# Kernel tuning notes

Measured on AMD Instinct MI355X. Metric: run time of the kernel, lower is better.

Reference implementation:

```python
import jax, jax.numpy as jnp
import numpy as np

B, N, E = 32, 1024, 768
H = 12
D = E // H  # head_dim = 64


def setup_inputs() -> dict:
    key = jax.random.key(0)
    ks = jax.random.split(key, 5)
    s = 0.02
    return {
        "x": jax.random.normal(ks[0], (B, N, E), dtype=jnp.float32),
        "w_qkv": jax.random.normal(ks[1], (E, 3 * E), dtype=jnp.float32) * s,
        "b_qkv": jax.random.normal(ks[2], (3 * E,), dtype=jnp.float32) * s,
        "w_proj": jax.random.normal(ks[3], (E, E), dtype=jnp.float32) * s,
        "b_proj": jax.random.normal(ks[4], (E,), dtype=jnp.float32) * s,
    }


def reference(x, w_qkv, b_qkv, w_proj, b_proj):
    b, n, e = x.shape
    # QKV projection -> [b, n, 3, H, D]
    qkv = (jnp.einsum('bne,ef->bnf', x, w_qkv) + b_qkv).reshape(b, n, 3, H, D)
    q = qkv[:, :, 0]  # [b, n, H, D]
    k = qkv[:, :, 1]
    v = qkv[:, :, 2]
    scale = 1.0 / jnp.sqrt(jnp.asarray(D, dtype=x.dtype))
    # attention scores [b, H, n, n]
    attn = jnp.einsum('bqhd,bkhd->bhqk', q, k) * scale
    attn = jax.nn.softmax(attn, axis=-1)
    # weighted values -> [b, n, H, D] -> [b, n, e]
    out = jnp.einsum('bhqk,bkhd->bqhd', attn, v).reshape(b, n, e)
    out = jnp.einsum('bne,ef->bnf', out, w_proj) + b_proj
    return out
```

## Files before the change

kernel.cpp:

```cpp
#include <hip/hip_runtime.h>
#include <hip/hip_bf16.h>
#include <stdint.h>

#define HB 12

typedef unsigned short u16;
typedef __bf16 bf16x8 __attribute__((ext_vector_type(8)));
typedef float f32x4 __attribute__((ext_vector_type(4)));
typedef float f4v __attribute__((ext_vector_type(4)));
typedef u16 u16x4 __attribute__((ext_vector_type(4)));
typedef u16 u16x8 __attribute__((ext_vector_type(8)));

__device__ __forceinline__ u16 f2bf(float f) {
  uint32_t u = __builtin_bit_cast(uint32_t, f);
  u += 0x7fffu + ((u >> 16) & 1u);
  return (u16)(u >> 16);
}

__device__ __forceinline__ void gld16(const u16* g, u16* l) {
  __builtin_amdgcn_global_load_lds((const __attribute__((address_space(1))) void*)g,
                                   (__attribute__((address_space(3))) void*)l, 16, 0, 0);
}

__device__ __forceinline__ f32x4 mfma_bf16(bf16x8 a, bf16x8 b, f32x4 c) {
  return __builtin_amdgcn_mfma_f32_16x16x32_bf16(a, b, c, 0, 0, 0);
}

__global__ void k_convert(const float* __restrict__ in, u16* __restrict__ out, int n4) {
  int stride = gridDim.x * blockDim.x;
  for (int i = blockIdx.x * blockDim.x + threadIdx.x; i < n4; i += stride) {
    f4v v = ((const f4v*)in)[i];
    u16x4 o;
    o[0] = f2bf(v[0]); o[1] = f2bf(v[1]); o[2] = f2bf(v[2]); o[3] = f2bf(v[3]);
    ((u16x4*)out)[i] = o;
  }
}

__global__ void k_transpose(const float* __restrict__ in, u16* __restrict__ out,
                            int rows, int cols) {
  __shared__ float t[32][33];
  int c0 = blockIdx.x * 32, r0 = blockIdx.y * 32;
  int tx = threadIdx.x, ty = threadIdx.y;
  for (int i = ty; i < 32; i += 8)
    t[i][tx] = in[(size_t)(r0 + i) * cols + c0 + tx];
  __syncthreads();
  for (int i = ty; i < 32; i += 8)
    out[(size_t)(c0 + i) * rows + r0 + tx] = f2bf(t[tx][i]);
}

template <int OUTF32>
__global__ void k_gemm(const u16* __restrict__ A, const u16* __restrict__ Bt,
                       const float* __restrict__ bias, void* __restrict__ C,
                       int Nc, int nx) {
  const int K = 768;
  __shared__ u16 lA[2][4096], lB[2][4096];
  int tid = threadIdx.x, w = tid >> 6, l = tid & 63;
  int lg = l >> 4, lr = l & 15;
  int wr = w >> 1, wc = w & 1;
  int lin = blockIdx.x;
  int xcd = lin & 7, idx = lin >> 3;
  int by = xcd * 32 + idx / nx;
  int bx = idx % nx;
  int m0 = by * 128, n0 = bx * 128;

  auto stage = [&](int buf, int k0) {
#pragma unroll
    for (int it = 0; it < 2; ++it) {
      int chunk = it * 256 + tid;
      int row = chunk >> 2, c = chunk & 3;
      int cg = (c ^ ((row >> 1) & 3)) * 8;
      gld16(&A[(size_t)(m0 + row) * K + k0 + cg], &lA[buf][chunk * 8]);
      gld16(&Bt[(size_t)(n0 + row) * K + k0 + cg], &lB[buf][chunk * 8]);
    }
  };

  f32x4 acc[4][4] = {};
  stage(0, 0);
  for (int kt = 0; kt < 24; ++kt) {
    __syncthreads();
    if (kt < 23) stage((kt + 1) & 1, (kt + 1) * 32);
    const u16* a = lA[kt & 1];
    const u16* b = lB[kt & 1];
    bf16x8 af[4], bfr[4];
#pragma unroll
    for (int i = 0; i < 4; ++i) {
      int ra = wr * 64 + i * 16 + lr;
      af[i] = *(const bf16x8*)&a[ra * 32 + ((lg ^ ((ra >> 1) & 3)) * 8)];
      int rb = wc * 64 + i * 16 + lr;
      bfr[i] = *(const bf16x8*)&b[rb * 32 + ((lg ^ ((rb >> 1) & 3)) * 8)];
    }
    __builtin_amdgcn_s_setprio(1);
#pragma unroll
    for (int i = 0; i < 4; ++i)
#pragma unroll
      for (int j = 0; j < 4; ++j)
        acc[i][j] = mfma_bf16(af[i], bfr[j], acc[i][j]);
    __builtin_amdgcn_s_setprio(0);
  }
#pragma unroll
  for (int j = 0; j < 4; ++j) {
    int col = n0 + wc * 64 + j * 16 + lr;
    float bv = bias[col];
#pragma unroll
    for (int i = 0; i < 4; ++i) {
      int rb = m0 + wr * 64 + i * 16 + lg * 4;
#pragma unroll
      for (int r = 0; r < 4; ++r) {
        float v = acc[i][j][r] + bv;
        if (OUTF32)
          ((float*)C)[(size_t)(rb + r) * Nc + col] = v;
        else
          ((u16*)C)[(size_t)(rb + r) * Nc + col] = f2bf(v);
      }
    }
  }
}

__global__ void k_vtrans(const u16* __restrict__ qkv, u16* __restrict__ vt) {
  __shared__ u16 t[64][80];
  int tid = threadIdx.x;
  int n0 = blockIdx.x * 64, bh = blockIdx.y;
  int b = bh / HB, h = bh % HB;
#pragma unroll
  for (int it = 0; it < 2; ++it) {
    int nl = it * 32 + (tid >> 3), dv0 = (tid & 7) * 8;
    u16x8 v = *(const u16x8*)&qkv[(size_t)(b * 1024 + n0 + nl) * 2304 + 1536 + h * 64 + dv0];
    *(u16x8*)&t[nl][dv0] = v;
  }
  __syncthreads();
  int dv = tid >> 2, c = (tid & 3) * 16;
  u16x8 o0, o1;
#pragma unroll
  for (int j = 0; j < 8; ++j) o0[j] = t[c + j][dv];
#pragma unroll
  for (int j = 0; j < 8; ++j) o1[j] = t[c + 8 + j][dv];
  size_t base = (size_t)(bh * 64 + dv) * 1024 + n0 + c;
  *(u16x8*)&vt[base] = o0;
  *(u16x8*)&vt[base + 8] = o1;
}

__global__ __launch_bounds__(256) void k_attn(const u16* __restrict__ qkv,
                                              const u16* __restrict__ vt,
                                              u16* __restrict__ out) {
  __shared__ u16 lK[2][4096];
  __shared__ u16 lV[2][4096];
  __shared__ u16 lP[8192];
  int tid = threadIdx.x, w = tid >> 6, l = tid & 63;
  int lg = l >> 4, lr = l & 15;
  int lin = blockIdx.x;
  int xcd = lin & 7, idx = lin >> 3;
  int bh = xcd * 48 + (idx >> 3);
  int qt = idx & 7;
  int b = bh / HB, h = bh % HB;
  int q0 = qt * 128;

#pragma unroll
  for (int it = 0; it < 4; ++it) {
    int chunk = it * 256 + tid;
    int row = chunk >> 3, c = chunk & 7;
    int cg = (c ^ (row & 7)) * 8;
    gld16(&qkv[(size_t)(b * 1024 + q0 + row) * 2304 + h * 64 + cg], &lP[chunk * 8]);
  }

  auto stage = [&](int buf, int kt) {
    int n0 = kt * 64;
#pragma unroll
    for (int it = 0; it < 2; ++it) {
      int chunk = it * 256 + tid;
      int row = chunk >> 3, c = chunk & 7;
      int cg = (c ^ (row & 7)) * 8;
      gld16(&qkv[(size_t)(b * 1024 + n0 + row) * 2304 + 768 + h * 64 + cg], &lK[buf][chunk * 8]);
      gld16(&vt[(size_t)(bh * 64 + row) * 1024 + n0 + cg], &lV[buf][chunk * 8]);
    }
  };

  stage(0, 0);
  __syncthreads();

  bf16x8 qf[2][2];
#pragma unroll
  for (int m = 0; m < 2; ++m)
#pragma unroll
    for (int kb = 0; kb < 2; ++kb) {
      int row = w * 32 + m * 16 + lr;
      qf[m][kb] = *(const bf16x8*)&lP[row * 64 + (((kb * 4 + lg) ^ (row & 7)) * 8)];
    }

  f32x4 oacc[2][4] = {};
  float mrun[2][4], lrun[2][4];
#pragma unroll
  for (int m = 0; m < 2; ++m)
#pragma unroll
    for (int j = 0; j < 4; ++j) { mrun[m][j] = -3.0e38f; lrun[m][j] = 0.f; }

  u16* Pw = &lP[w * 2048];
  const float scale = 0.125f;

  for (int kt = 0; kt < 16; ++kt) {
    int cur = kt & 1;
    if (kt < 15) stage(cur ^ 1, kt + 1);
    const u16* Kc = lK[cur];
    const u16* Vc = lV[cur];

    f32x4 sacc[2][4] = {};
    __builtin_amdgcn_s_setprio(1);
#pragma unroll
    for (int nf = 0; nf < 4; ++nf) {
      int rk = nf * 16 + lr;
      bf16x8 k0 = *(const bf16x8*)&Kc[rk * 64 + ((lg ^ (rk & 7)) * 8)];
      bf16x8 k1 = *(const bf16x8*)&Kc[rk * 64 + (((4 + lg) ^ (rk & 7)) * 8)];
      sacc[0][nf] = mfma_bf16(qf[0][0], k0, sacc[0][nf]);
      sacc[0][nf] = mfma_bf16(qf[0][1], k1, sacc[0][nf]);
      sacc[1][nf] = mfma_bf16(qf[1][0], k0, sacc[1][nf]);
      sacc[1][nf] = mfma_bf16(qf[1][1], k1, sacc[1][nf]);
    }
    __builtin_amdgcn_s_setprio(0);

#pragma unroll
    for (int m = 0; m < 2; ++m) {
#pragma unroll
      for (int j = 0; j < 4; ++j) {
        float tmax = -3.0e38f;
#pragma unroll
        for (int nf = 0; nf < 4; ++nf) {
          sacc[m][nf][j] *= scale;
          tmax = fmaxf(tmax, sacc[m][nf][j]);
        }
        tmax = fmaxf(tmax, __shfl_xor(tmax, 1));
        tmax = fmaxf(tmax, __shfl_xor(tmax, 2));
        tmax = fmaxf(tmax, __shfl_xor(tmax, 4));
        tmax = fmaxf(tmax, __shfl_xor(tmax, 8));
        float mnew = fmaxf(mrun[m][j], tmax);
        float corr = __expf(mrun[m][j] - mnew);
        float rsum = 0.f;
#pragma unroll
        for (int nf = 0; nf < 4; ++nf) {
          float p = __expf(sacc[m][nf][j] - mnew);
          sacc[m][nf][j] = p;
          rsum += p;
        }
        rsum += __shfl_xor(rsum, 1);
        rsum += __shfl_xor(rsum, 2);
        rsum += __shfl_xor(rsum, 4);
        rsum += __shfl_xor(rsum, 8);
        lrun[m][j] = lrun[m][j] * corr + rsum;
        mrun[m][j] = mnew;
#pragma unroll
        for (int dvf = 0; dvf < 4; ++dvf) oacc[m][dvf][j] *= corr;
      }
    }

#pragma unroll
    for (int m = 0; m < 2; ++m)
#pragma unroll
      for (int nf = 0; nf < 4; ++nf)
#pragma unroll
        for (int j = 0; j < 4; ++j) {
          int row = m * 16 + lg * 4 + j;
          int col = nf * 16 + lr;
          Pw[row * 64 + (((col >> 3) ^ (row & 7)) * 8) + (col & 7)] = f2bf(sacc[m][nf][j]);
        }

    __builtin_amdgcn_s_setprio(1);
#pragma unroll
    for (int kb2 = 0; kb2 < 2; ++kb2) {
      bf16x8 pf0, pf1;
      {
        int c = kb2 * 4 + lg;
        int r0r = lr;
        pf0 = *(const bf16x8*)&Pw[r0r * 64 + ((c ^ (r0r & 7)) * 8)];
        int r1r = 16 + lr;
        pf1 = *(const bf16x8*)&Pw[r1r * 64 + ((c ^ (r1r & 7)) * 8)];
      }
#pragma unroll
      for (int dvf = 0; dvf < 4; ++dvf) {
        int rv = dvf * 16 + lr, c = kb2 * 4 + lg;
        bf16x8 vf = *(const bf16x8*)&Vc[rv * 64 + ((c ^ (rv & 7)) * 8)];
        oacc[0][dvf] = mfma_bf16(pf0, vf, oacc[0][dvf]);
        oacc[1][dvf] = mfma_bf16(pf1, vf, oacc[1][dvf]);
      }
    }
    __builtin_amdgcn_s_setprio(0);

    if (kt < 15) __syncthreads();
  }

#pragma unroll
  for (int m = 0; m < 2; ++m)
#pragma unroll
    for (int j = 0; j < 4; ++j) {
      float inv = 1.f / lrun[m][j];
      int q = q0 + w * 32 + m * 16 + lg * 4 + j;
#pragma unroll
      for (int dvf = 0; dvf < 4; ++dvf) {
        int dv = dvf * 16 + lr;
        out[(size_t)(b * 1024 + q) * 768 + h * 64 + dv] = f2bf(oacc[m][dvf][j] * inv);
      }
    }
}

extern "C" void kernel_launch(void* const* d_in, const int* in_sizes, int n_in,
                              void* d_out, int out_size, void* d_ws, size_t ws_size,
                              hipStream_t stream) {
  const float* x      = (const float*)d_in[0];
  const float* w_qkv  = (const float*)d_in[1];
  const float* b_qkv  = (const float*)d_in[2];
  const float* w_proj = (const float*)d_in[3];
  const float* b_proj = (const float*)d_in[4];

  u16* ws = (u16*)d_ws;
  u16* xbf    = ws;
  u16* attn_o = xbf;
  u16* wqkvT  = ws + 25165824;
  u16* wprojT = wqkvT + 1769472;
  u16* qkvb   = wprojT + 589824;
  u16* vtb    = qkvb + 75497472;

  k_convert<<<2048, 256, 0, stream>>>(x, xbf, 25165824 / 4);
  k_transpose<<<dim3(2304 / 32, 768 / 32), dim3(32, 8), 0, stream>>>(w_qkv, wqkvT, 768, 2304);
  k_transpose<<<dim3(768 / 32, 768 / 32), dim3(32, 8), 0, stream>>>(w_proj, wprojT, 768, 768);
  k_gemm<0><<<18 * 256, 256, 0, stream>>>(xbf, wqkvT, b_qkv, qkvb, 2304, 18);
  k_vtrans<<<dim3(16, 384), 256, 0, stream>>>(qkvb, vtb);
  k_attn<<<3072, 256, 0, stream>>>(qkvb, vtb, attn_o);
  k_gemm<1><<<6 * 256, 256, 0, stream>>>(attn_o, wprojT, b_proj, d_out, 768, 6);
}
```

Before: 720.3 us.

## Switch attention to 32x32 MFMA with transposed S, keep P in registers

After: 584.2 us. -18.9%, faster.

```diff
diff --git a/kernel.cpp b/kernel.cpp
--- a/kernel.cpp
+++ b/kernel.cpp
@@ -5,17 +5,24 @@
 #define HB 12
 
 typedef unsigned short u16;
+typedef unsigned int u32;
 typedef __bf16 bf16x8 __attribute__((ext_vector_type(8)));
 typedef float f32x4 __attribute__((ext_vector_type(4)));
+typedef float f32x16 __attribute__((ext_vector_type(16)));
 typedef float f4v __attribute__((ext_vector_type(4)));
 typedef u16 u16x4 __attribute__((ext_vector_type(4)));
 typedef u16 u16x8 __attribute__((ext_vector_type(8)));
+typedef u32 u32x2 __attribute__((ext_vector_type(2)));
+typedef u32 u32x4v __attribute__((ext_vector_type(4)));
 
 __device__ __forceinline__ u16 f2bf(float f) {
   uint32_t u = __builtin_bit_cast(uint32_t, f);
   u += 0x7fffu + ((u >> 16) & 1u);
   return (u16)(u >> 16);
 }
+__device__ __forceinline__ u32 pack2bf(float lo, float hi) {
+  return (u32)f2bf(lo) | ((u32)f2bf(hi) << 16);
+}
 
 __device__ __forceinline__ void gld16(const u16* g, u16* l) {
   __builtin_amdgcn_global_load_lds((const __attribute__((address_space(1))) void*)g,
@@ -24,6 +31,9 @@
 
 __device__ __forceinline__ f32x4 mfma_bf16(bf16x8 a, bf16x8 b, f32x4 c) {
   return __builtin_amdgcn_mfma_f32_16x16x32_bf16(a, b, c, 0, 0, 0);
+}
+__device__ __forceinline__ f32x16 mfma32(bf16x8 a, bf16x8 b, f32x16 c) {
+  return __builtin_amdgcn_mfma_f32_32x32x16_bf16(a, b, c, 0, 0, 0);
 }
 
 __global__ void k_convert(const float* __restrict__ in, u16* __restrict__ out, int n4) {
@@ -139,27 +149,25 @@
   *(u16x8*)&vt[base + 8] = o1;
 }
 
-__global__ __launch_bounds__(256) void k_attn(const u16* __restrict__ qkv,
-                                              const u16* __restrict__ vt,
-                                              u16* __restrict__ out) {
+__global__ __launch_bounds__(256, 4) void k_attn(const u16* __restrict__ qkv,
+                                                 const u16* __restrict__ vt,
+                                                 u16* __restrict__ out) {
   __shared__ u16 lK[2][4096];
   __shared__ u16 lV[2][4096];
-  __shared__ u16 lP[8192];
   int tid = threadIdx.x, w = tid >> 6, l = tid & 63;
-  int lg = l >> 4, lr = l & 15;
+  int q32 = l & 31, hi = l >> 5;
   int lin = blockIdx.x;
   int xcd = lin & 7, idx = lin >> 3;
   int bh = xcd * 48 + (idx >> 3);
   int qt = idx & 7;
   int b = bh / HB, h = bh % HB;
-  int q0 = qt * 128;
-
-#pragma unroll
-  for (int it = 0; it < 4; ++it) {
-    int chunk = it * 256 + tid;
-    int row = chunk >> 3, c = chunk & 7;
-    int cg = (c ^ (row & 7)) * 8;
-    gld16(&qkv[(size_t)(b * 1024 + q0 + row) * 2304 + h * 64 + cg], &lP[chunk * 8]);
+  int qg = qt * 128 + w * 32 + q32;
+
+  bf16x8 qf[4];
+  {
+    const u16* qrow = &qkv[(size_t)(b * 1024 + qg) * 2304 + h * 64 + hi * 8];
+#pragma unroll
+    for (int ds = 0; ds < 4; ++ds) qf[ds] = *(const bf16x8*)&qrow[ds * 16];
   }
 
   auto stage = [&](int buf, int kt) {
@@ -177,24 +185,8 @@
   stage(0, 0);
   __syncthreads();
 
-  bf16x8 qf[2][2];
-#pragma unroll
-  for (int m = 0; m < 2; ++m)
-#pragma unroll
-    for (int kb = 0; kb < 2; ++kb) {
-      int row = w * 32 + m * 16 + lr;
-      qf[m][kb] = *(const bf16x8*)&lP[row * 64 + (((kb * 4 + lg) ^ (row & 7)) * 8)];
-    }
-
-  f32x4 oacc[2][4] = {};
-  float mrun[2][4], lrun[2][4];
-#pragma unroll
-  for (int m = 0; m < 2; ++m)
-#pragma unroll
-    for (int j = 0; j < 4; ++j) { mrun[m][j] = -3.0e38f; lrun[m][j] = 0.f; }
-
-  u16* Pw = &lP[w * 2048];
-  const float scale = 0.125f;
+  f32x16 oacc[2] = {};
+  float mrun = -3.0e38f, lrun = 0.f;
 
   for (int kt = 0; kt < 16; ++kt) {
     int cur = kt & 1;
@@ -202,100 +194,86 @@
     const u16* Kc = lK[cur];
     const u16* Vc = lV[cur];
 
-    f32x4 sacc[2][4] = {};
+    f32x16 s0 = {}, s1 = {};
     __builtin_amdgcn_s_setprio(1);
 #pragma unroll
-    for (int nf = 0; nf < 4; ++nf) {
-      int rk = nf * 16 + lr;
-      bf16x8 k0 = *(const bf16x8*)&Kc[rk * 64 + ((lg ^ (rk & 7)) * 8)];
-      bf16x8 k1 = *(const bf16x8*)&Kc[rk * 64 + (((4 + lg) ^ (rk & 7)) * 8)];
-      sacc[0][nf] = mfma_bf16(qf[0][0], k0, sacc[0][nf]);
-      sacc[0][nf] = mfma_bf16(qf[0][1], k1, sacc[0][nf]);
-      sacc[1][nf] = mfma_bf16(qf[1][0], k0, sacc[1][nf]);
-      sacc[1][nf] = mfma_bf16(qf[1][1], k1, sacc[1][nf]);
+    for (int ds = 0; ds < 4; ++ds) {
+      int dchunk = ds * 2 + hi;
+      int r0 = q32;
+      bf16x8 k0 = *(const bf16x8*)&Kc[r0 * 64 + ((dchunk ^ (r0 & 7)) * 8)];
+      int r1 = 32 + q32;
+      bf16x8 k1 = *(const bf16x8*)&Kc[r1 * 64 + ((dchunk ^ (r1 & 7)) * 8)];
+      s0 = mfma32(k0, qf[ds], s0);
+      s1 = mfma32(k1, qf[ds], s1);
     }
     __builtin_amdgcn_s_setprio(0);
 
-#pragma unroll
-    for (int m = 0; m < 2; ++m) {
-#pragma unroll
-      for (int j = 0; j < 4; ++j) {
-        float tmax = -3.0e38f;
-#pragma unroll
-        for (int nf = 0; nf < 4; ++nf) {
-          sacc[m][nf][j] *= scale;
-          tmax = fmaxf(tmax, sacc[m][nf][j]);
+    float tmax = -3.0e38f;
+#pragma unroll
+    for (int r = 0; r < 16; ++r) { s0[r] *= 0.125f; tmax = fmaxf(tmax, s0[r]); }
+#pragma unroll
+    for (int r = 0; r < 16; ++r) { s1[r] *= 0.125f; tmax = fmaxf(tmax, s1[r]); }
+    tmax = fmaxf(tmax, __shfl_xor(tmax, 32));
+
+    float mnew = fmaxf(mrun, tmax);
+    float corr = __expf(mrun - mnew);
+    lrun *= corr;
+#pragma unroll
+    for (int r = 0; r < 16; ++r) { oacc[0][r] *= corr; oacc[1][r] *= corr; }
+    mrun = mnew;
+
+    float rsum = 0.f;
+#pragma unroll
+    for (int r = 0; r < 16; ++r) { float p = __expf(s0[r] - mnew); s0[r] = p; rsum += p; }
+#pragma unroll
+    for (int r = 0; r < 16; ++r) { float p = __expf(s1[r] - mnew); s1[r] = p; rsum += p; }
+    lrun += rsum + __shfl_xor(rsum, 32);
+
+    __builtin_amdgcn_s_setprio(1);
+#pragma unroll
+    for (int half = 0; half < 2; ++half) {
+      const f32x16& pv = half ? s1 : s0;
+#pragma unroll
+      for (int u = 0; u < 2; ++u) {
+        int ns = half * 2 + u;
+        u32 a0 = pack2bf(pv[8 * u + 0], pv[8 * u + 1]);
+        u32 a1 = pack2bf(pv[8 * u + 2], pv[8 * u + 3]);
+        u32 a2 = pack2bf(pv[8 * u + 4], pv[8 * u + 5]);
+        u32 a3 = pack2bf(pv[8 * u + 6], pv[8 * u + 7]);
+        u32 pa0 = (u32)__shfl_xor((int)a0, 32);
+        u32 pa1 = (u32)__shfl_xor((int)a1, 32);
+        u32 pa2 = (u32)__shfl_xor((int)a2, 32);
+        u32 pa3 = (u32)__shfl_xor((int)a3, 32);
+        u32x4v pw;
+        pw[0] = hi ? pa2 : a0;
+        pw[1] = hi ? pa3 : a1;
+        pw[2] = hi ? a2 : pa0;
+        pw[3] = hi ? a3 : pa1;
+        bf16x8 pfrag = __builtin_bit_cast(bf16x8, pw);
+        int nchunk = ns * 2 + hi;
+#pragma unroll
+        for (int dt = 0; dt < 2; ++dt) {
+          int rv = dt * 32 + q32;
+          bf16x8 vf = *(const bf16x8*)&Vc[rv * 64 + ((nchunk ^ (rv & 7)) * 8)];
+          oacc[dt] = mfma32(vf, pfrag, oacc[dt]);
         }
-        tmax = fmaxf(tmax, __shfl_xor(tmax, 1));
-        tmax = fmaxf(tmax, __shfl_xor(tmax, 2));
-        tmax = fmaxf(tmax, __shfl_xor(tmax, 4));
-        tmax = fmaxf(tmax, __shfl_xor(tmax, 8));
-        float mnew = fmaxf(mrun[m][j], tmax);
-        float corr = __expf(mrun[m][j] - mnew);
-        float rsum = 0.f;
-#pragma unroll
-        for (int nf = 0; nf < 4; ++nf) {
-          float p = __expf(sacc[m][nf][j] - mnew);
-          sacc[m][nf][j] = p;
-          rsum += p;
-        }
-        rsum += __shfl_xor(rsum, 1);
-        rsum += __shfl_xor(rsum, 2);
-        rsum += __shfl_xor(rsum, 4);
-        rsum += __shfl_xor(rsum, 8);
-        lrun[m][j] = lrun[m][j] * corr + rsum;
-        mrun[m][j] = mnew;
-#pragma unroll
-        for (int dvf = 0; dvf < 4; ++dvf) oacc[m][dvf][j] *= corr;
       }
     }
-
-#pragma unroll
-    for (int m = 0; m < 2; ++m)
-#pragma unroll
-      for (int nf = 0; nf < 4; ++nf)
-#pragma unroll
-        for (int j = 0; j < 4; ++j) {
-          int row = m * 16 + lg * 4 + j;
-          int col = nf * 16 + lr;
-          Pw[row * 64 + (((col >> 3) ^ (row & 7)) * 8) + (col & 7)] = f2bf(sacc[m][nf][j]);
-        }
-
-    __builtin_amdgcn_s_setprio(1);
-#pragma unroll
-    for (int kb2 = 0; kb2 < 2; ++kb2) {
-      bf16x8 pf0, pf1;
-      {
-        int c = kb2 * 4 + lg;
-        int r0r = lr;
-        pf0 = *(const bf16x8*)&Pw[r0r * 64 + ((c ^ (r0r & 7)) * 8)];
-        int r1r = 16 + lr;
-        pf1 = *(const bf16x8*)&Pw[r1r * 64 + ((c ^ (r1r & 7)) * 8)];
-      }
-#pragma unroll
-      for (int dvf = 0; dvf < 4; ++dvf) {
-        int rv = dvf * 16 + lr, c = kb2 * 4 + lg;
-        bf16x8 vf = *(const bf16x8*)&Vc[rv * 64 + ((c ^ (rv & 7)) * 8)];
-        oacc[0][dvf] = mfma_bf16(pf0, vf, oacc[0][dvf]);
-        oacc[1][dvf] = mfma_bf16(pf1, vf, oacc[1][dvf]);
-      }
-    }
     __builtin_amdgcn_s_setprio(0);
 
     if (kt < 15) __syncthreads();
   }
 
-#pragma unroll
-  for (int m = 0; m < 2; ++m)
-#pragma unroll
-    for (int j = 0; j < 4; ++j) {
-      float inv = 1.f / lrun[m][j];
-      int q = q0 + w * 32 + m * 16 + lg * 4 + j;
-#pragma unroll
-      for (int dvf = 0; dvf < 4; ++dvf) {
-        int dv = dvf * 16 + lr;
-        out[(size_t)(b * 1024 + q) * 768 + h * 64 + dv] = f2bf(oacc[m][dvf][j] * inv);
-      }
+  float inv = 1.0f / lrun;
+  u16* orow = &out[(size_t)(b * 1024 + qg) * 768 + h * 64 + hi * 4];
+#pragma unroll
+  for (int dt = 0; dt < 2; ++dt)
+#pragma unroll
+    for (int g = 0; g < 4; ++g) {
+      u32 wa = pack2bf(oacc[dt][4 * g + 0] * inv, oacc[dt][4 * g + 1] * inv);
+      u32 wb = pack2bf(oacc[dt][4 * g + 2] * inv, oacc[dt][4 * g + 3] * inv);
+      u32x2 pr; pr[0] = wa; pr[1] = wb;
+      *(u32x2*)&orow[dt * 32 + g * 8] = pr;
     }
 }
 
```
